# Kernel tuning notes

Hardware: AMD Instinct MI355X
Metric: run time of the kernel (lower is better)

## Reference

```python
import jax, jax.numpy as jnp
import numpy as np

B, L, D, F, T = 32, 768, 256, 256, 3072
_EPS = 1e-5


def _layernorm(h, g, b):
    mu = jnp.mean(h, axis=-1, keepdims=True)
    var = jnp.var(h, axis=-1, keepdims=True)
    return (h - mu) * jax.lax.rsqrt(var + _EPS) * g + b


def _conv1d(h, w, b):
    # h: [B, L, Cin], w: [K, Cin, Cout] (HIO), padding=1 matches torch Conv1d(padding=1)
    return jax.lax.conv_general_dilated(h, w, (1,), [(1, 1)], dimension_numbers=('NHC', 'HIO', 'NHC')) + b


def setup_inputs() -> dict:
    key = jax.random.key(0)
    ks = jax.random.split(key, 6)
    return {
        'x': jax.random.normal(ks[0], (B, L, D), jnp.float32),
        'target': jax.random.randint(ks[1], (B, L), 0, 4, jnp.int32),
        'mel_max_length': T,
        'conv1_w': jax.random.normal(ks[2], (3, D, F), jnp.float32) * 0.05,
        'conv1_b': jnp.zeros((F,), jnp.float32),
        'ln1_g': jnp.ones((F,), jnp.float32),
        'ln1_b': jnp.zeros((F,), jnp.float32),
        'conv2_w': jax.random.normal(ks[3], (3, F, F), jnp.float32) * 0.05,
        'conv2_b': jnp.zeros((F,), jnp.float32),
        'ln2_g': jnp.ones((F,), jnp.float32),
        'ln2_b': jnp.zeros((F,), jnp.float32),
        'lin_w': jax.random.normal(ks[4], (F, 1), jnp.float32) * 0.05,
        'lin_b': jnp.zeros((1,), jnp.float32),
    }


def reference(x, target, mel_max_length, conv1_w, conv1_b, ln1_g, ln1_b,
              conv2_w, conv2_b, ln2_g, ln2_b, lin_w, lin_b):
    alpha = 1.0
    # DurationPredictor: conv -> relu -> LN -> conv -> relu -> LN -> linear (dropout=0)
    h = _layernorm(jax.nn.relu(_conv1d(x, conv1_w, conv1_b)), ln1_g, ln1_b)
    h = _layernorm(jax.nn.relu(_conv1d(h, conv2_w, conv2_b)), ln2_g, ln2_b)
    dp_out = (h @ lin_w + lin_b)[..., 0]                       # [B, L]
    durations = jnp.exp(dp_out) * alpha                        # [B, L] float
    # Training branch: durations come from target
    dpo = jnp.round(target.astype(jnp.float32) * alpha).astype(jnp.int32)  # [B, L]
    # LR: alignment @ x realized as cumulative-duration searchsorted + gather
    cum = jnp.cumsum(dpo, axis=1)                              # [B, L]
    t = jnp.arange(mel_max_length, dtype=jnp.int32)            # [T]
    idx = jax.vmap(lambda c: jnp.searchsorted(c, t, side='right'))(cum)  # [B, T]
    mask = (t[None, :] < cum[:, -1:]).astype(x.dtype)          # [B, T] zero past total frames
    out = jnp.take_along_axis(x, jnp.clip(idx, 0, x.shape[1] - 1)[:, :, None], axis=1)
    out = out * mask[:, :, None]                               # [B, T, D]
    return (out, dpo, durations)
```

## Files before the change

kernel.cpp:

```cpp
#include <hip/hip_runtime.h>
#include <hip/hip_bf16.h>
#include <math.h>

#define BB 32
#define LL 768
#define DD 256
#define FF 256
#define TT 3072
#define MT 48
#define PAD 262
#define A1R 66

typedef __attribute__((ext_vector_type(8))) short bf16x8;
typedef __attribute__((ext_vector_type(4))) float f32x4;

__device__ inline unsigned short f2b(float f) {
    union { float f; unsigned u; } v; v.f = f;
    unsigned r = (v.u + 0x7FFF + ((v.u >> 16) & 1)) >> 16;
    return (unsigned short)r;
}

#define DPP_ROR_ADD(v, ctrl)                                                   \
    v += __int_as_float(__builtin_amdgcn_update_dpp(                           \
        0, __float_as_int(v), ctrl, 0xF, 0xF, false))

__device__ inline void red16_pair(float& a, float& b) {
    DPP_ROR_ADD(a, 0x128); DPP_ROR_ADD(b, 0x128);
    DPP_ROR_ADD(a, 0x124); DPP_ROR_ADD(b, 0x124);
    DPP_ROR_ADD(a, 0x122); DPP_ROR_ADD(b, 0x122);
    DPP_ROR_ADD(a, 0x121); DPP_ROR_ADD(b, 0x121);
}

__device__ inline float red16_one(float a) {
    DPP_ROR_ADD(a, 0x128);
    DPP_ROR_ADD(a, 0x124);
    DPP_ROR_ADD(a, 0x122);
    DPP_ROR_ADD(a, 0x121);
    return a;
}

__global__ __launch_bounds__(256) void prep_w_kernel(
    const float* __restrict__ w1, const float* __restrict__ w2,
    unsigned short* __restrict__ wQ1, unsigned short* __restrict__ wQ2)
{
    const int layer = blockIdx.x / 24;
    const int s  = blockIdx.x % 24;
    const int kc = s >> 3, c8 = s & 7;
    const float* __restrict__ w = layer ? w2 : w1;
    unsigned short* __restrict__ o = (layer ? wQ2 : wQ1) + s * 8192 + threadIdx.x * 32;
    const int n = threadIdx.x;

    alignas(16) unsigned short tmp[32];
#pragma unroll
    for (int q = 0; q < 4; ++q)
#pragma unroll
        for (int j = 0; j < 8; ++j) {
            const int cin = c8 * 32 + q * 8 + j;
            tmp[q * 8 + j] = f2b(w[((size_t)(kc * 256 + cin)) * 256 + n]);
        }
#pragma unroll
    for (int i = 0; i < 4; ++i)
        *reinterpret_cast<uint4*>(o + i * 8) = *reinterpret_cast<const uint4*>(tmp + i * 8);
}

__global__ __launch_bounds__(256) void fused_dp_kernel(
    const float* __restrict__ x,
    const unsigned short* __restrict__ wQ1,
    const unsigned short* __restrict__ wQ2,
    const float* __restrict__ c1b, const float* __restrict__ g1, const float* __restrict__ b1,
    const float* __restrict__ c2b, const float* __restrict__ g2, const float* __restrict__ b2,
    const float* __restrict__ lw,  const float* __restrict__ lb,
    float* __restrict__ out_dur)
{
    __shared__ union {
        unsigned short A1[A1R * PAD];
        unsigned short h2[50 * PAD];
    } sm;
    __shared__ float red[4][4][4][4][2];
    __shared__ float redp[4][3][4][4];
    __shared__ float fin[50][2];

    const int tid  = threadIdx.x;
    const int b    = blockIdx.x / (LL / MT);
    const int l0   = (blockIdx.x % (LL / MT)) * MT;
    const int wave = tid >> 6, lane = tid & 63;
    const int quad = lane >> 4, l16 = lane & 15;

    int   cols[4];
    float c1bv[4], g1v[4], b1v[4], c2bv[4], g2v[4], b2v[4], lwv[4];
#pragma unroll
    for (int nt = 0; nt < 4; ++nt) {
        const int c = wave * 64 + nt * 16 + l16;
        cols[nt] = c;
        c1bv[nt] = c1b[c]; g1v[nt] = g1[c]; b1v[nt] = b1[c];
        c2bv[nt] = c2b[c]; g2v[nt] = g2[c]; b2v[nt] = b2[c];
        lwv[nt]  = lw[c];
    }
    const float lbv = lb[0];

    {
        const int ch = (tid & 31) * 8;
        const int rr = tid >> 5;
        for (int p = 0; p < 9; ++p) {
            const int ar = p * 8 + rr;
            if (ar >= A1R) break;
            const int l = l0 - 2 + ar;
            bf16x8 val;
#pragma unroll
            for (int j = 0; j < 8; ++j) val[j] = 0;
            if (ar < 52 && l >= 0 && l < LL) {
                const float* pp = x + ((size_t)b * LL + l) * DD + ch;
                const float4 v0 = *reinterpret_cast<const float4*>(pp);
                const float4 v1 = *reinterpret_cast<const float4*>(pp + 4);
                val[0] = (short)f2b(v0.x); val[1] = (short)f2b(v0.y);
                val[2] = (short)f2b(v0.z); val[3] = (short)f2b(v0.w);
                val[4] = (short)f2b(v1.x); val[5] = (short)f2b(v1.y);
                val[6] = (short)f2b(v1.z); val[7] = (short)f2b(v1.w);
            }
            *reinterpret_cast<bf16x8*>(&sm.A1[ar * PAD + ch]) = val;
        }
    }
    __syncthreads();

    f32x4 acc1[4][4] = {};
    for (int s = 0; s < 24; ++s) {
        const int kc = s >> 3, c8 = s & 7;
        bf16x8 a[4], bf[4];
#pragma unroll
        for (int mt = 0; mt < 4; ++mt)
            a[mt] = *reinterpret_cast<const bf16x8*>(
                &sm.A1[(16 * mt + l16 + kc) * PAD + c8 * 32 + quad * 8]);
#pragma unroll
        for (int nt = 0; nt < 4; ++nt)
            bf[nt] = *reinterpret_cast<const bf16x8*>(
                wQ1 + (size_t)s * 8192 + cols[nt] * 32 + quad * 8);
#pragma unroll
        for (int mt = 0; mt < 4; ++mt)
#pragma unroll
            for (int nt = 0; nt < 4; ++nt)
                acc1[mt][nt] = __builtin_amdgcn_mfma_f32_16x16x32_bf16(
                    a[mt], bf[nt], acc1[mt][nt], 0, 0, 0);
    }
    __syncthreads();

#pragma unroll
    for (int mt = 0; mt < 4; ++mt)
#pragma unroll
        for (int r = 0; r < 4; ++r) {
            float s1 = 0.f, s2 = 0.f;
#pragma unroll
            for (int nt = 0; nt < 4; ++nt) {
                const float v = fmaxf(acc1[mt][nt][r] + c1bv[nt], 0.f);
                s1 += v; s2 += v * v;
            }
            red16_pair(s1, s2);
            if (l16 == 0) { red[wave][mt][quad][r][0] = s1; red[wave][mt][quad][r][1] = s2; }
        }
    __syncthreads();
    if (tid < 50) {
        const int mt = tid >> 4, q = (tid >> 2) & 3, r = tid & 3;
        const float s1 = red[0][mt][q][r][0] + red[1][mt][q][r][0]
                       + red[2][mt][q][r][0] + red[3][mt][q][r][0];
        const float s2 = red[0][mt][q][r][1] + red[1][mt][q][r][1]
                       + red[2][mt][q][r][1] + red[3][mt][q][r][1];
        const float mu  = s1 * (1.f / 256.f);
        const float var = s2 * (1.f / 256.f) - mu * mu;
        fin[tid][0] = mu;
        fin[tid][1] = rsqrtf(var + 1e-5f);
    }
    __syncthreads();

#pragma unroll
    for (int mt = 0; mt < 4; ++mt)
#pragma unroll
        for (int r = 0; r < 4; ++r) {
            const int rho = 16 * mt + quad * 4 + r;
            if (rho < 50) {
                const int gr = l0 - 1 + rho;
                const float mu = fin[rho][0], rstd = fin[rho][1];
#pragma unroll
                for (int nt = 0; nt < 4; ++nt) {
                    unsigned short hv = 0;
                    if (gr >= 0 && gr < LL) {
                        const float v = fmaxf(acc1[mt][nt][r] + c1bv[nt], 0.f);
                        hv = f2b((v - mu) * rstd * g1v[nt] + b1v[nt]);
                    }
                    sm.h2[rho * PAD + cols[nt]] = hv;
                }
            }
        }
    __syncthreads();

    f32x4 acc2[3][4] = {};
    for (int s = 0; s < 24; ++s) {
        const int kc = s >> 3, c8 = s & 7;
        bf16x8 a[3], bf[4];
#pragma unroll
        for (int mt = 0; mt < 3; ++mt)
            a[mt] = *reinterpret_cast<const bf16x8*>(
                &sm.h2[(16 * mt + l16 + kc) * PAD + c8 * 32 + quad * 8]);
#pragma unroll
        for (int nt = 0; nt < 4; ++nt)
            bf[nt] = *reinterpret_cast<const bf16x8*>(
                wQ2 + (size_t)s * 8192 + cols[nt] * 32 + quad * 8);
#pragma unroll
        for (int mt = 0; mt < 3; ++mt)
#pragma unroll
            for (int nt = 0; nt < 4; ++nt)
                acc2[mt][nt] = __builtin_amdgcn_mfma_f32_16x16x32_bf16(
                    a[mt], bf[nt], acc2[mt][nt], 0, 0, 0);
    }

#pragma unroll
    for (int mt = 0; mt < 3; ++mt)
#pragma unroll
        for (int r = 0; r < 4; ++r) {
            float s1 = 0.f, s2 = 0.f;
#pragma unroll
            for (int nt = 0; nt < 4; ++nt) {
                const float v = fmaxf(acc2[mt][nt][r] + c2bv[nt], 0.f);
                s1 += v; s2 += v * v;
            }
            red16_pair(s1, s2);
            if (l16 == 0) { red[wave][mt][quad][r][0] = s1; red[wave][mt][quad][r][1] = s2; }
        }
    __syncthreads();
    if (tid < MT) {
        const int mt = tid >> 4, q = (tid >> 2) & 3, r = tid & 3;
        const float s1 = red[0][mt][q][r][0] + red[1][mt][q][r][0]
                       + red[2][mt][q][r][0] + red[3][mt][q][r][0];
        const float s2 = red[0][mt][q][r][1] + red[1][mt][q][r][1]
                       + red[2][mt][q][r][1] + red[3][mt][q][r][1];
        const float mu  = s1 * (1.f / 256.f);
        const float var = s2 * (1.f / 256.f) - mu * mu;
        fin[tid][0] = mu;
        fin[tid][1] = rsqrtf(var + 1e-5f);
    }
    __syncthreads();

#pragma unroll
    for (int mt = 0; mt < 3; ++mt)
#pragma unroll
        for (int r = 0; r < 4; ++r) {
            const int rho = 16 * mt + quad * 4 + r;
            const float mu = fin[rho][0], rstd = fin[rho][1];
            float p = 0.f;
#pragma unroll
            for (int nt = 0; nt < 4; ++nt) {
                const float v = fmaxf(acc2[mt][nt][r] + c2bv[nt], 0.f);
                p += ((v - mu) * rstd * g2v[nt] + b2v[nt]) * lwv[nt];
            }
            p = red16_one(p);
            if (l16 == 0) redp[wave][mt][quad][r] = p;
        }
    __syncthreads();
    if (tid < MT) {
        const int mt = tid >> 4, q = (tid >> 2) & 3, r = tid & 3;
        const float dp = redp[0][mt][q][r] + redp[1][mt][q][r]
                       + redp[2][mt][q][r] + redp[3][mt][q][r] + lbv;
        out_dur[(size_t)b * LL + l0 + tid] = expf(dp);
    }
}

__global__ __launch_bounds__(256) void scan_kernel(
    const int* __restrict__ target,
    float* __restrict__ out_dpo,
    int* __restrict__ idx_map)
{
    __shared__ int tsum[256];
    const int b = blockIdx.x, tid = threadIdx.x;

    const int l = 3 * tid;
    const int v0 = target[b * LL + l];
    const int v1 = target[b * LL + l + 1];
    const int v2 = target[b * LL + l + 2];
    out_dpo[b * LL + l]     = (float)v0;
    out_dpo[b * LL + l + 1] = (float)v1;
    out_dpo[b * LL + l + 2] = (float)v2;

    const int s0 = v0, s1 = v0 + v1, s2 = v0 + v1 + v2;
    tsum[tid] = s2;
    __syncthreads();
    for (int off = 1; off < 256; off <<= 1) {
        int xq = (tid >= off) ? tsum[tid - off] : 0;
        __syncthreads();
        tsum[tid] += xq;
        __syncthreads();
    }
    const int excl = tsum[tid] - s2;

    for (int t = tid; t < TT; t += 256) idx_map[b * TT + t] = -1;
    __syncthreads();

    const int c0 = excl + s0, c1 = excl + s1, c2 = excl + s2;
    for (int t = excl; t < c0 && t < TT; ++t) idx_map[b * TT + t] = l;
    for (int t = c0;   t < c1 && t < TT; ++t) idx_map[b * TT + t] = l + 1;
    for (int t = c1;   t < c2 && t < TT; ++t) idx_map[b * TT + t] = l + 2;
}

__global__ __launch_bounds__(256) void gather_kernel(
    const float* __restrict__ x,
    const int* __restrict__ idx_map,
    float* __restrict__ out)
{
    const int wv = threadIdx.x >> 6, lane = threadIdx.x & 63;
    const int row = blockIdx.x * 4 + wv;
    const int b = row / TT, t = row - b * TT;
    const int idx = idx_map[b * TT + t];
    f32x4 val = {0.f, 0.f, 0.f, 0.f};
    if (idx >= 0)
        val = *reinterpret_cast<const f32x4*>(x + ((size_t)(b * LL + idx)) * DD + lane * 4);
    __builtin_nontemporal_store(val, reinterpret_cast<f32x4*>(out) + (size_t)row * (DD / 4) + lane);
}

extern "C" void kernel_launch(void* const* d_in, const int* in_sizes, int n_in,
                              void* d_out, int out_size, void* d_ws, size_t ws_size,
                              hipStream_t stream)
{
    const float* x      = (const float*)d_in[0];
    const int*   target = (const int*)  d_in[1];
    const float* c1w = (const float*)d_in[3];
    const float* c1b = (const float*)d_in[4];
    const float* g1  = (const float*)d_in[5];
    const float* b1  = (const float*)d_in[6];
    const float* c2w = (const float*)d_in[7];
    const float* c2b = (const float*)d_in[8];
    const float* g2  = (const float*)d_in[9];
    const float* b2  = (const float*)d_in[10];
    const float* lw  = (const float*)d_in[11];
    const float* lb  = (const float*)d_in[12];

    float* out0    = (float*)d_out;
    float* out_dpo = out0 + (size_t)BB * TT * DD;
    float* out_dur = out_dpo + (size_t)BB * LL;

    char* ws = (char*)d_ws;
    unsigned short* wQ1 = (unsigned short*)ws;                 ws += (size_t)24 * 8192 * 2;
    unsigned short* wQ2 = (unsigned short*)ws;                 ws += (size_t)24 * 8192 * 2;
    int* idx_map        = (int*)ws;

    prep_w_kernel<<<48, 256, 0, stream>>>(c1w, c2w, wQ1, wQ2);

    fused_dp_kernel<<<BB * (LL / MT), 256, 0, stream>>>(
        x, wQ1, wQ2, c1b, g1, b1, c2b, g2, b2, lw, lb, out_dur);

    scan_kernel<<<BB, 256, 0, stream>>>(target, out_dpo, idx_map);
    gather_kernel<<<BB * TT / 4, 256, 0, stream>>>(x, idx_map, out0);
}
```

Measured before the change: 199.4 us.

## Merge scan into weight prep, double-buffer MFMA operand loads, batch x loads

Folds the per-batch scan kernel into the weight-prep kernel as extra blocks, which removes one launch and lets the scan run alongside the weight conversion. The two conv GEMM loops now use even/odd register buffers, so the loads for the next K-step are issued before the current MFMAs. The input tile loads are batched into registers before the bf16 conversion and LDS stores, with the padding rows zeroed separately. Adding launch_bounds(256,2) together with the extra operand registers may raise register pressure or cause spills.

```diff
diff --git a/kernel.cpp b/kernel.cpp
--- a/kernel.cpp
+++ b/kernel.cpp
@@ -39,31 +39,69 @@
     return a;
 }
 
-__global__ __launch_bounds__(256) void prep_w_kernel(
+__global__ __launch_bounds__(256) void prep_scan_kernel(
     const float* __restrict__ w1, const float* __restrict__ w2,
-    unsigned short* __restrict__ wQ1, unsigned short* __restrict__ wQ2)
+    unsigned short* __restrict__ wQ1, unsigned short* __restrict__ wQ2,
+    const int* __restrict__ target,
+    float* __restrict__ out_dpo,
+    int* __restrict__ idx_map)
 {
-    const int layer = blockIdx.x / 24;
-    const int s  = blockIdx.x % 24;
-    const int kc = s >> 3, c8 = s & 7;
-    const float* __restrict__ w = layer ? w2 : w1;
-    unsigned short* __restrict__ o = (layer ? wQ2 : wQ1) + s * 8192 + threadIdx.x * 32;
-    const int n = threadIdx.x;
-
-    alignas(16) unsigned short tmp[32];
-#pragma unroll
-    for (int q = 0; q < 4; ++q)
-#pragma unroll
-        for (int j = 0; j < 8; ++j) {
-            const int cin = c8 * 32 + q * 8 + j;
-            tmp[q * 8 + j] = f2b(w[((size_t)(kc * 256 + cin)) * 256 + n]);
-        }
-#pragma unroll
-    for (int i = 0; i < 4; ++i)
-        *reinterpret_cast<uint4*>(o + i * 8) = *reinterpret_cast<const uint4*>(tmp + i * 8);
-}
-
-__global__ __launch_bounds__(256) void fused_dp_kernel(
+    __shared__ int tsum[256];
+    const int tid = threadIdx.x;
+
+    if (blockIdx.x < 48) {
+        const int layer = blockIdx.x / 24;
+        const int s  = blockIdx.x % 24;
+        const int kc = s >> 3, c8 = s & 7;
+        const float* __restrict__ w = layer ? w2 : w1;
+        unsigned short* __restrict__ o = (layer ? wQ2 : wQ1) + s * 8192 + tid * 32;
+        const int n = tid;
+
+        alignas(16) unsigned short tmp[32];
+#pragma unroll
+        for (int q = 0; q < 4; ++q)
+#pragma unroll
+            for (int j = 0; j < 8; ++j) {
+                const int cin = c8 * 32 + q * 8 + j;
+                tmp[q * 8 + j] = f2b(w[((size_t)(kc * 256 + cin)) * 256 + n]);
+            }
+#pragma unroll
+        for (int i = 0; i < 4; ++i)
+            *reinterpret_cast<uint4*>(o + i * 8) = *reinterpret_cast<const uint4*>(tmp + i * 8);
+        return;
+    }
+
+    const int b = blockIdx.x - 48;
+
+    const int l = 3 * tid;
+    const int v0 = target[b * LL + l];
+    const int v1 = target[b * LL + l + 1];
+    const int v2 = target[b * LL + l + 2];
+    out_dpo[b * LL + l]     = (float)v0;
+    out_dpo[b * LL + l + 1] = (float)v1;
+    out_dpo[b * LL + l + 2] = (float)v2;
+
+    const int s0 = v0, s1 = v0 + v1, s2 = v0 + v1 + v2;
+    tsum[tid] = s2;
+    __syncthreads();
+    for (int off = 1; off < 256; off <<= 1) {
+        int xq = (tid >= off) ? tsum[tid - off] : 0;
+        __syncthreads();
+        tsum[tid] += xq;
+        __syncthreads();
+    }
+    const int excl = tsum[tid] - s2;
+
+    for (int t = tid; t < TT; t += 256) idx_map[b * TT + t] = -1;
+    __syncthreads();
+
+    const int c0 = excl + s0, c1 = excl + s1, c2 = excl + s2;
+    for (int t = excl; t < c0 && t < TT; ++t) idx_map[b * TT + t] = l;
+    for (int t = c0;   t < c1 && t < TT; ++t) idx_map[b * TT + t] = l + 1;
+    for (int t = c1;   t < c2 && t < TT; ++t) idx_map[b * TT + t] = l + 2;
+}
+
+__global__ __launch_bounds__(256, 2) void fused_dp_kernel(
     const float* __restrict__ x,
     const unsigned short* __restrict__ wQ1,
     const unsigned short* __restrict__ wQ2,
@@ -99,47 +137,74 @@
     const float lbv = lb[0];
 
     {
-        const int ch = (tid & 31) * 8;
-        const int rr = tid >> 5;
-        for (int p = 0; p < 9; ++p) {
-            const int ar = p * 8 + rr;
-            if (ar >= A1R) break;
-            const int l = l0 - 2 + ar;
+        float4 v0[7], v1[7];
+        int lr[7];
+#pragma unroll
+        for (int k = 0; k < 7; ++k) {
+            const int q  = tid + (k << 8);
+            const int ar = q >> 5;
+            const int l  = l0 - 2 + ar;
+            lr[k] = (ar < 52 && l >= 0 && l < LL) ? l : -1;
+            if (lr[k] >= 0) {
+                const float* pp = x + ((size_t)b * LL + lr[k]) * DD + (q & 31) * 8;
+                v0[k] = *reinterpret_cast<const float4*>(pp);
+                v1[k] = *reinterpret_cast<const float4*>(pp + 4);
+            }
+        }
+#pragma unroll
+        for (int k = 0; k < 7; ++k) {
+            const int q  = tid + (k << 8);
+            const int ar = q >> 5;
             bf16x8 val;
 #pragma unroll
             for (int j = 0; j < 8; ++j) val[j] = 0;
-            if (ar < 52 && l >= 0 && l < LL) {
-                const float* pp = x + ((size_t)b * LL + l) * DD + ch;
-                const float4 v0 = *reinterpret_cast<const float4*>(pp);
-                const float4 v1 = *reinterpret_cast<const float4*>(pp + 4);
-                val[0] = (short)f2b(v0.x); val[1] = (short)f2b(v0.y);
-                val[2] = (short)f2b(v0.z); val[3] = (short)f2b(v0.w);
-                val[4] = (short)f2b(v1.x); val[5] = (short)f2b(v1.y);
-                val[6] = (short)f2b(v1.z); val[7] = (short)f2b(v1.w);
-            }
-            *reinterpret_cast<bf16x8*>(&sm.A1[ar * PAD + ch]) = val;
+            if (lr[k] >= 0) {
+                val[0] = (short)f2b(v0[k].x); val[1] = (short)f2b(v0[k].y);
+                val[2] = (short)f2b(v0[k].z); val[3] = (short)f2b(v0[k].w);
+                val[4] = (short)f2b(v1[k].x); val[5] = (short)f2b(v1[k].y);
+                val[6] = (short)f2b(v1[k].z); val[7] = (short)f2b(v1[k].w);
+            }
+            *reinterpret_cast<bf16x8*>(&sm.A1[ar * PAD + (q & 31) * 8]) = val;
+        }
+        for (int q = tid; q < 320; q += 256) {
+            const int ar = 56 + (q >> 5);
+            bf16x8 z;
+#pragma unroll
+            for (int j = 0; j < 8; ++j) z[j] = 0;
+            *reinterpret_cast<bf16x8*>(&sm.A1[ar * PAD + (q & 31) * 8]) = z;
         }
     }
     __syncthreads();
 
     f32x4 acc1[4][4] = {};
-    for (int s = 0; s < 24; ++s) {
-        const int kc = s >> 3, c8 = s & 7;
-        bf16x8 a[4], bf[4];
-#pragma unroll
-        for (int mt = 0; mt < 4; ++mt)
-            a[mt] = *reinterpret_cast<const bf16x8*>(
-                &sm.A1[(16 * mt + l16 + kc) * PAD + c8 * 32 + quad * 8]);
-#pragma unroll
-        for (int nt = 0; nt < 4; ++nt)
-            bf[nt] = *reinterpret_cast<const bf16x8*>(
-                wQ1 + (size_t)s * 8192 + cols[nt] * 32 + quad * 8);
-#pragma unroll
-        for (int mt = 0; mt < 4; ++mt)
+    {
+        bf16x8 aE[4], bE[4], aO[4], bO[4];
+        auto ld1 = [&](bf16x8* a, bf16x8* bf, int s) {
+            const int kc = s >> 3, c8 = s & 7;
+#pragma unroll
+            for (int mt = 0; mt < 4; ++mt)
+                a[mt] = *reinterpret_cast<const bf16x8*>(
+                    &sm.A1[(16 * mt + l16 + kc) * PAD + c8 * 32 + quad * 8]);
 #pragma unroll
             for (int nt = 0; nt < 4; ++nt)
-                acc1[mt][nt] = __builtin_amdgcn_mfma_f32_16x16x32_bf16(
-                    a[mt], bf[nt], acc1[mt][nt], 0, 0, 0);
+                bf[nt] = *reinterpret_cast<const bf16x8*>(
+                    wQ1 + (size_t)s * 8192 + cols[nt] * 32 + quad * 8);
+        };
+        auto mm1 = [&](bf16x8* a, bf16x8* bf) {
+#pragma unroll
+            for (int mt = 0; mt < 4; ++mt)
+#pragma unroll
+                for (int nt = 0; nt < 4; ++nt)
+                    acc1[mt][nt] = __builtin_amdgcn_mfma_f32_16x16x32_bf16(
+                        a[mt], bf[nt], acc1[mt][nt], 0, 0, 0);
+        };
+        ld1(aE, bE, 0);
+        for (int s = 0; s < 24; s += 2) {
+            ld1(aO, bO, s + 1);
+            mm1(aE, bE);
+            if (s + 2 < 24) ld1(aE, bE, s + 2);
+            mm1(aO, bO);
+        }
     }
     __syncthreads();
 
@@ -192,23 +257,34 @@
     __syncthreads();
 
     f32x4 acc2[3][4] = {};
-    for (int s = 0; s < 24; ++s) {
-        const int kc = s >> 3, c8 = s & 7;
-        bf16x8 a[3], bf[4];
-#pragma unroll
-        for (int mt = 0; mt < 3; ++mt)
-            a[mt] = *reinterpret_cast<const bf16x8*>(
-                &sm.h2[(16 * mt + l16 + kc) * PAD + c8 * 32 + quad * 8]);
-#pragma unroll
-        for (int nt = 0; nt < 4; ++nt)
-            bf[nt] = *reinterpret_cast<const bf16x8*>(
-                wQ2 + (size_t)s * 8192 + cols[nt] * 32 + quad * 8);
-#pragma unroll
-        for (int mt = 0; mt < 3; ++mt)
+    {
+        bf16x8 aE[3], bE[4], aO[3], bO[4];
+        auto ld2 = [&](bf16x8* a, bf16x8* bf, int s) {
+            const int kc = s >> 3, c8 = s & 7;
+#pragma unroll
+            for (int mt = 0; mt < 3; ++mt)
+                a[mt] = *reinterpret_cast<const bf16x8*>(
+                    &sm.h2[(16 * mt + l16 + kc) * PAD + c8 * 32 + quad * 8]);
 #pragma unroll
             for (int nt = 0; nt < 4; ++nt)
-                acc2[mt][nt] = __builtin_amdgcn_mfma_f32_16x16x32_bf16(
-                    a[mt], bf[nt], acc2[mt][nt], 0, 0, 0);
+                bf[nt] = *reinterpret_cast<const bf16x8*>(
+                    wQ2 + (size_t)s * 8192 + cols[nt] * 32 + quad * 8);
+        };
+        auto mm2 = [&](bf16x8* a, bf16x8* bf) {
+#pragma unroll
+            for (int mt = 0; mt < 3; ++mt)
+#pragma unroll
+                for (int nt = 0; nt < 4; ++nt)
+                    acc2[mt][nt] = __builtin_amdgcn_mfma_f32_16x16x32_bf16(
+                        a[mt], bf[nt], acc2[mt][nt], 0, 0, 0);
+        };
+        ld2(aE, bE, 0);
+        for (int s = 0; s < 24; s += 2) {
+            ld2(aO, bO, s + 1);
+            mm2(aE, bE);
+            if (s + 2 < 24) ld2(aE, bE, s + 2);
+            mm2(aO, bO);
+        }
     }
 
 #pragma unroll
@@ -260,42 +336,6 @@
                        + redp[2][mt][q][r] + redp[3][mt][q][r] + lbv;
         out_dur[(size_t)b * LL + l0 + tid] = expf(dp);
     }
-}
-
-__global__ __launch_bounds__(256) void scan_kernel(
-    const int* __restrict__ target,
-    float* __restrict__ out_dpo,
-    int* __restrict__ idx_map)
-{
-    __shared__ int tsum[256];
-    const int b = blockIdx.x, tid = threadIdx.x;
-
-    const int l = 3 * tid;
-    const int v0 = target[b * LL + l];
-    const int v1 = target[b * LL + l + 1];
-    const int v2 = target[b * LL + l + 2];
-    out_dpo[b * LL + l]     = (float)v0;
-    out_dpo[b * LL + l + 1] = (float)v1;
-    out_dpo[b * LL + l + 2] = (float)v2;
-
-    const int s0 = v0, s1 = v0 + v1, s2 = v0 + v1 + v2;
-    tsum[tid] = s2;
-    __syncthreads();
-    for (int off = 1; off < 256; off <<= 1) {
-        int xq = (tid >= off) ? tsum[tid - off] : 0;
-        __syncthreads();
-        tsum[tid] += xq;
-        __syncthreads();
-    }
-    const int excl = tsum[tid] - s2;
-
-    for (int t = tid; t < TT; t += 256) idx_map[b * TT + t] = -1;
-    __syncthreads();
-
-    const int c0 = excl + s0, c1 = excl + s1, c2 = excl + s2;
-    for (int t = excl; t < c0 && t < TT; ++t) idx_map[b * TT + t] = l;
-    for (int t = c0;   t < c1 && t < TT; ++t) idx_map[b * TT + t] = l + 1;
-    for (int t = c1;   t < c2 && t < TT; ++t) idx_map[b * TT + t] = l + 2;
 }
 
 __global__ __launch_bounds__(256) void gather_kernel(
@@ -339,11 +379,11 @@
     unsigned short* wQ2 = (unsigned short*)ws;                 ws += (size_t)24 * 8192 * 2;
     int* idx_map        = (int*)ws;
 
-    prep_w_kernel<<<48, 256, 0, stream>>>(c1w, c2w, wQ1, wQ2);
+    prep_scan_kernel<<<48 + BB, 256, 0, stream>>>(
+        c1w, c2w, wQ1, wQ2, target, out_dpo, idx_map);
 
     fused_dp_kernel<<<BB * (LL / MT), 256, 0, stream>>>(
         x, wQ1, wQ2, c1b, g1, b1, c2b, g2, b2, lw, lb, out_dur);
 
-    scan_kernel<<<BB, 256, 0, stream>>>(target, out_dpo, idx_map);
     gather_kernel<<<BB * TT / 4, 256, 0, stream>>>(x, idx_map, out0);
 }
```

Result: faster. 195.3 us (-2.0%).
